# Performance work log

Hardware: AMD Instinct MI355X
Metric: run time of the kernel (lower is better)

## Reference

```python
import jax, jax.numpy as jnp
import numpy as np

B, NQ, NK, D_IN, HD = 1, 16384, 7933, 1024, 512
R = 0.3  # keep-top-r fraction used for the quantile threshold


def _l2norm(x):
    # matches F.normalize(p=2, dim=-1, eps=1e-12)
    n = jnp.linalg.norm(x, axis=-1, keepdims=True)
    return x / jnp.maximum(n, 1e-12)


def setup_inputs() -> dict:
    key = jax.random.key(0)
    ks = jax.random.split(key, 10)
    s = 0.02
    return {
        "query": jax.random.normal(ks[0], (B, NQ, D_IN), jnp.float32),
        "key_x": jax.random.normal(ks[1], (B, NK, D_IN), jnp.float32),
        "wq_w": jax.random.normal(ks[2], (HD, D_IN), jnp.float32) * s,
        "wq_b": jnp.zeros((HD,), jnp.float32),
        "wk_w": jax.random.normal(ks[3], (HD, D_IN), jnp.float32) * s,
        "wk_b": jnp.zeros((HD,), jnp.float32),
        "wa_w": jax.random.normal(ks[4], (1, NK), jnp.float32) * s,
        "wa_b": jnp.zeros((1,), jnp.float32),
        "cls_w": jax.random.normal(ks[5], (1, HD), jnp.float32) * s,
        "cls_b": jnp.zeros((1,), jnp.float32),
    }


def reference(query, key_x, wq_w, wq_b, wk_w, wk_b, wa_w, wa_b, cls_w, cls_b):
    # WQ / WK: Linear + Tanh
    q = jnp.tanh(jnp.einsum("bnd,hd->bnh", query, wq_w) + wq_b)   # [B,NQ,HD]
    k = jnp.tanh(jnp.einsum("bnd,hd->bnh", key_x, wk_w) + wk_b)   # [B,NK,HD]
    # normalized dot-product scores
    A = jnp.einsum("bqh,bkh->bqk", _l2norm(q), _l2norm(k))        # [B,NQ,NK]
    # WA: Linear(NK -> 1)
    A1 = jnp.einsum("bqk,ok->bqo", A, wa_w) + wa_b                # [B,NQ,1]
    # quantile threshold from batch 0 (torch: sorted ascending, index -int(r*NQ))
    thre = jax.lax.stop_gradient(jnp.sort(A1[0, :, 0])[-int(R * NQ)])
    A1 = jnp.where(A1 > thre, A1, 0.0)                            # F.threshold(., thre, 0)
    attn = jax.nn.softmax(A1, axis=1)                             # softmax over NQ (zeros included)
    attn_t = jnp.transpose(attn, (0, 2, 1))                       # [B,1,NQ]
    z = jnp.matmul(attn_t, q).reshape(-1, HD)                     # [B,HD]
    y_prob = z @ cls_w.T + cls_b                                  # [B,1]
    return (y_prob, attn_t)
```

## Files before the change

### kernel.cpp

```cpp
#include <hip/hip_runtime.h>
#include <math.h>

#define NQ 16384
#define NK 7933
#define DI 1024
#define HD 512
#define RANK_TARGET 11469

typedef __bf16 bf16x8 __attribute__((ext_vector_type(8)));
typedef float  f32x4  __attribute__((ext_vector_type(4)));

#define GLOAD_LDS16(g, l)                                                     \
  __builtin_amdgcn_global_load_lds(                                           \
      (const __attribute__((address_space(1))) void*)(g),                     \
      (__attribute__((address_space(3))) void*)(l), 16, 0, 0)

__device__ __forceinline__ unsigned mapf(float f) {
  unsigned b = __float_as_uint(f);
  return (b & 0x80000000u) ? ~b : (b | 0x80000000u);
}

__global__ void conv_all(const float* __restrict__ q, const float* __restrict__ k,
                         const float* __restrict__ wq, const float* __restrict__ wk,
                         __bf16* __restrict__ qbf, __bf16* __restrict__ kbf,
                         __bf16* __restrict__ wqbf, __bf16* __restrict__ wkbf,
                         unsigned* __restrict__ zero_region) {
  if (blockIdx.x == 0) {
    for (int j = threadIdx.x; j < 1088; j += 256) zero_region[j] = 0u;
  }
  const int NQ8 = NQ * DI / 8;
  const int NK8 = NK * DI / 8;
  const int W8  = HD * DI / 8;
  const int total = NQ8 + NK8 + 2 * W8;
  int i = blockIdx.x * blockDim.x + threadIdx.x;
  int stride = gridDim.x * blockDim.x;
  for (; i < total; i += stride) {
    const float* s; __bf16* d; int j;
    if (i < NQ8)                 { s = q;  d = qbf;  j = i; }
    else if (i < NQ8 + NK8)      { s = k;  d = kbf;  j = i - NQ8; }
    else if (i < NQ8 + NK8 + W8) { s = wq; d = wqbf; j = i - NQ8 - NK8; }
    else                         { s = wk; d = wkbf; j = i - NQ8 - NK8 - W8; }
    float4 a = ((const float4*)s)[2 * j];
    float4 b = ((const float4*)s)[2 * j + 1];
    bf16x8 o;
    o[0] = (__bf16)a.x; o[1] = (__bf16)a.y; o[2] = (__bf16)a.z; o[3] = (__bf16)a.w;
    o[4] = (__bf16)b.x; o[5] = (__bf16)b.y; o[6] = (__bf16)b.z; o[7] = (__bf16)b.w;
    ((bf16x8*)d)[j] = o;
  }
}

template <bool FUSE_A1>
__global__ __launch_bounds__(256, 3)
void gemm_bt_tanh(const __bf16* __restrict__ A, const __bf16* __restrict__ B,
                  const float* __restrict__ bias, float* __restrict__ C, int M,
                  const float* __restrict__ v, float* __restrict__ A1dot,
                  float* __restrict__ A1ss) {
  constexpr int K = DI;
  constexpr int N = HD;
  __shared__ __align__(16) __bf16 sA[128 * 64];
  __shared__ __align__(16) __bf16 sB[128 * 64];

  const int tid  = threadIdx.x;
  const int lane = tid & 63;
  const int wave = tid >> 6;
  const int wr = wave >> 1, wc = wave & 1;
  const int m0 = blockIdx.x * 128, n0 = blockIdx.y * 128;

  const int srow = lane >> 3;
  const int scol = (((lane & 7) ^ srow)) << 3;

  const int lrow = lane & 15;
  const int chi  = lane >> 4;

  f32x4 acc[4][4] = {};

  for (int kk = 0; kk < K; kk += 64) {
    __syncthreads();
#pragma unroll
    for (int c = 0; c < 4; ++c) {
      int seg = wave * 4 + c;
      int row = seg * 8 + srow;
      int ga = m0 + row; if (ga > M - 1) ga = M - 1;
      GLOAD_LDS16(A + (size_t)ga * K + kk + scol, &sA[seg * 512]);
      GLOAD_LDS16(B + (size_t)(n0 + row) * K + kk + scol, &sB[seg * 512]);
    }
    __syncthreads();
#pragma unroll
    for (int ks = 0; ks < 64; ks += 32) {
      const int cc = (ks >> 3) + chi;
      const int sw = ((cc ^ (lrow & 7)) << 3);
      bf16x8 af[4], bfr[4];
#pragma unroll
      for (int mi = 0; mi < 4; ++mi)
        af[mi] = *(const bf16x8*)(&sA[(wr * 64 + mi * 16 + lrow) * 64 + sw]);
#pragma unroll
      for (int ni = 0; ni < 4; ++ni)
        bfr[ni] = *(const bf16x8*)(&sB[(wc * 64 + ni * 16 + lrow) * 64 + sw]);
#pragma unroll
      for (int mi = 0; mi < 4; ++mi)
#pragma unroll
        for (int ni = 0; ni < 4; ++ni)
          acc[mi][ni] = __builtin_amdgcn_mfma_f32_16x16x32_bf16(af[mi], bfr[ni], acc[mi][ni], 0, 0, 0);
    }
  }

  const int rbase = m0 + wr * 64 + ((lane >> 4) << 2);
  const int cbase = n0 + wc * 64 + (lane & 15);
  float b4[4], v4[4];
#pragma unroll
  for (int ni = 0; ni < 4; ++ni) {
    b4[ni] = bias[cbase + ni * 16];
    if constexpr (FUSE_A1) v4[ni] = v[cbase + ni * 16];
  }
#pragma unroll
  for (int mi = 0; mi < 4; ++mi) {
#pragma unroll
    for (int r = 0; r < 4; ++r) {
      int grow = rbase + mi * 16 + r;
      if (grow < M) {
        float pd = 0.f, pss = 0.f;
#pragma unroll
        for (int ni = 0; ni < 4; ++ni) {
          float val = tanhf(acc[mi][ni][r] + b4[ni]);
          C[(size_t)grow * N + cbase + ni * 16] = val;
          if constexpr (FUSE_A1) { pd += val * v4[ni]; pss += val * val; }
        }
        if constexpr (FUSE_A1) {
#pragma unroll
          for (int off = 1; off < 16; off <<= 1) {
            pd += __shfl_xor(pd, off);
            pss += __shfl_xor(pss, off);
          }
          if ((lane & 15) == 0) {
            atomicAdd(&A1dot[grow], pd);
            atomicAdd(&A1ss[grow], pss);
          }
        }
      }
    }
  }
}

__global__ __launch_bounds__(256)
void reduce_v_zero(const float* __restrict__ kt, const float* __restrict__ wa,
                   float* __restrict__ v, int M, uint2* __restrict__ zr) {
  {
    int g = blockIdx.x * 256 + threadIdx.x;
    uint2 zz; zz.x = 0u; zz.y = 0u;
    zr[g] = zz;
    if (g < 24576 - 16384) zr[16384 + g] = zz;
  }
  __shared__ float vpart[4][512];
  const int tid = threadIdx.x, lane = tid & 63, wave = tid >> 6;
  const int gw = blockIdx.x * 4 + wave;
  const int tw = gridDim.x * 4;
  float acc[8] = {0, 0, 0, 0, 0, 0, 0, 0};
  for (int r = gw; r < M; r += tw) {
    const float4* p = (const float4*)(kt + (size_t)r * HD + lane * 8);
    float4 x = p[0], y = p[1];
    float ss = x.x * x.x + x.y * x.y + x.z * x.z + x.w * x.w
             + y.x * y.x + y.y * y.y + y.z * y.z + y.w * y.w;
#pragma unroll
    for (int off = 32; off; off >>= 1) ss += __shfl_xor(ss, off);
    float s = wa[r] / fmaxf(sqrtf(ss), 1e-12f);
    acc[0] += s * x.x; acc[1] += s * x.y; acc[2] += s * x.z; acc[3] += s * x.w;
    acc[4] += s * y.x; acc[5] += s * y.y; acc[6] += s * y.z; acc[7] += s * y.w;
  }
#pragma unroll
  for (int j = 0; j < 8; ++j) vpart[wave][lane * 8 + j] = acc[j];
  __syncthreads();
  for (int c = tid; c < 512; c += 256)
    atomicAdd(&v[c], vpart[0][c] + vpart[1][c] + vpart[2][c] + vpart[3][c]);
}

__global__ __launch_bounds__(1024)
void select_kernel(const float* __restrict__ A1dot, const float* __restrict__ A1ss,
                   const float* __restrict__ wa_b, float* __restrict__ A1,
                   unsigned* __restrict__ keyg, float* __restrict__ scf) {
  __shared__ unsigned wred1[16], wred2[16], wred3[16];
  __shared__ unsigned s_res;
  const int t = threadIdx.x, lane = t & 63, wave = t >> 6;
  const float wab = wa_b[0];
  unsigned kloc[16];
#pragma unroll 4
  for (int j = 0; j < 16; ++j) {
    int i = j * 1024 + t;
    float d = A1dot[i], ss = A1ss[i];
    float a1 = d / fmaxf(sqrtf(ss), 1e-12f) + wab;
    A1[i] = a1;
    unsigned k = mapf(a1);
    kloc[j] = k;
    keyg[i] = k;
  }
  if (t == 0) s_res = 0u;
  __syncthreads();

  for (int b = 30; b >= 0; b -= 2) {
    const unsigned res = s_res;
    const unsigned t1 = res | (1u << b);
    const unsigned t2 = res | (2u << b);
    const unsigned t3 = res | (3u << b);
    unsigned c1 = 0, c2 = 0, c3 = 0;
#pragma unroll
    for (int j = 0; j < 16; ++j) {
      unsigned k = kloc[j];
      c1 += (k < t1); c2 += (k < t2); c3 += (k < t3);
    }
#pragma unroll
    for (int off = 32; off; off >>= 1) {
      c1 += __shfl_xor(c1, off);
      c2 += __shfl_xor(c2, off);
      c3 += __shfl_xor(c3, off);
    }
    if (lane == 0) { wred1[wave] = c1; wred2[wave] = c2; wred3[wave] = c3; }
    __syncthreads();
    if (t == 0) {
      unsigned C1 = 0, C2 = 0, C3 = 0;
      for (int w = 0; w < 16; ++w) { C1 += wred1[w]; C2 += wred2[w]; C3 += wred3[w]; }
      unsigned nr = res;
      if (C3 <= RANK_TARGET)      nr = t3;
      else if (C2 <= RANK_TARGET) nr = t2;
      else if (C1 <= RANK_TARGET) nr = t1;
      s_res = nr;
    }
    __syncthreads();
  }
  if (t == 0) {
    unsigned key = s_res;
    unsigned bits = (key & 0x80000000u) ? (key ^ 0x80000000u) : ~key;
    scf[0] = __uint_as_float(bits);
  }
}

__global__ __launch_bounds__(256)
void expz(const float* __restrict__ A1, const float* __restrict__ qt,
          float* __restrict__ scf, float* __restrict__ e_out,
          float* __restrict__ z) {
  __shared__ float vpart[4][512];
  __shared__ float esum[4];
  const int tid = threadIdx.x, lane = tid & 63, wave = tid >> 6;
  const float thre = scf[0];
  const int gw = blockIdx.x * 4 + wave;
  const int tw = gridDim.x * 4;
  float acc[8] = {0, 0, 0, 0, 0, 0, 0, 0};
  float es = 0.f;
  for (int r = gw; r < NQ; r += tw) {
    float x = A1[r]; x = (x > thre) ? x : 0.f;
    float e = expf(x - thre);
    if (lane == 0) e_out[r] = e;
    es += e;
    const float4* p = (const float4*)(qt + (size_t)r * HD + lane * 8);
    float4 u = p[0], w = p[1];
    acc[0] += e * u.x; acc[1] += e * u.y; acc[2] += e * u.z; acc[3] += e * u.w;
    acc[4] += e * w.x; acc[5] += e * w.y; acc[6] += e * w.z; acc[7] += e * w.w;
  }
  if (lane == 0) esum[wave] = es;
#pragma unroll
  for (int j = 0; j < 8; ++j) vpart[wave][lane * 8 + j] = acc[j];
  __syncthreads();
  for (int c = tid; c < 512; c += 256)
    atomicAdd(&z[c], vpart[0][c] + vpart[1][c] + vpart[2][c] + vpart[3][c]);
  if (tid == 0) atomicAdd(&scf[2], esum[0] + esum[1] + esum[2] + esum[3]);
}

__global__ __launch_bounds__(256)
void finalize(float* __restrict__ attn, const float* __restrict__ scf,
              const float* __restrict__ z, const float* __restrict__ cls_w,
              const float* __restrict__ cls_b, float* __restrict__ y) {
  const float invZ = 1.f / scf[2];
  if (blockIdx.x < 64) {
    int i = blockIdx.x * 256 + threadIdx.x;
    attn[i] *= invZ;
  } else if (threadIdx.x < 64) {
    const int lane = threadIdx.x;
    const float4* zp = (const float4*)(z + lane * 8);
    const float4* wp = (const float4*)(cls_w + lane * 8);
    float4 a = zp[0], b = zp[1], c = wp[0], d = wp[1];
    float dot = a.x * c.x + a.y * c.y + a.z * c.z + a.w * c.w
              + b.x * d.x + b.y * d.y + b.z * d.z + b.w * d.w;
#pragma unroll
    for (int off = 32; off; off >>= 1) dot += __shfl_xor(dot, off);
    if (lane == 0) y[0] = dot * invZ + cls_b[0];
  }
}

#define OFF_WQBF 0u
#define OFF_WKBF 1048576u
#define OFF_A1D  1048576u
#define OFF_A1S  1114112u
#define OFF_KEY  1179648u
#define OFF_QBF  2097152u
#define OFF_A1   35651584u
#define OFF_V    35717120u
#define OFF_Z    35719168u
#define OFF_SC   35721216u
#define OFF_KBF  35721472u
#define OFF_KT   51968256u
#define OFF_QT   35721472u

extern "C" void kernel_launch(void* const* d_in, const int* in_sizes, int n_in,
                              void* d_out, int out_size, void* d_ws, size_t ws_size,
                              hipStream_t stream) {
  const float* query = (const float*)d_in[0];
  const float* key_x = (const float*)d_in[1];
  const float* wq_w  = (const float*)d_in[2];
  const float* wq_b  = (const float*)d_in[3];
  const float* wk_w  = (const float*)d_in[4];
  const float* wk_b  = (const float*)d_in[5];
  const float* wa_w  = (const float*)d_in[6];
  const float* wa_b  = (const float*)d_in[7];
  const float* cls_w = (const float*)d_in[8];
  const float* cls_b = (const float*)d_in[9];
  float* out = (float*)d_out;

  char* ws = (char*)d_ws;
  __bf16* wqbf  = (__bf16*)(ws + OFF_WQBF);
  __bf16* wkbf  = (__bf16*)(ws + OFF_WKBF);
  float*  A1dot = (float*)(ws + OFF_A1D);
  float*  A1ss  = (float*)(ws + OFF_A1S);
  unsigned* keyg = (unsigned*)(ws + OFF_KEY);
  __bf16* qbf   = (__bf16*)(ws + OFF_QBF);
  float*  A1    = (float*)(ws + OFF_A1);
  float*  v     = (float*)(ws + OFF_V);
  float*  z     = (float*)(ws + OFF_Z);
  float*  scf   = (float*)(ws + OFF_SC);
  __bf16* kbf   = (__bf16*)(ws + OFF_KBF);
  float*  ktanh = (float*)(ws + OFF_KT);
  float*  qtanh = (float*)(ws + OFF_QT);
  float*  out_attn = out + 1;

  conv_all<<<4096, 256, 0, stream>>>(query, key_x, wq_w, wk_w,
                                     qbf, kbf, wqbf, wkbf, (unsigned*)v);

  gemm_bt_tanh<false><<<dim3(62, 4), 256, 0, stream>>>(
      kbf, wkbf, wk_b, ktanh, NK, nullptr, nullptr, nullptr);

  reduce_v_zero<<<64, 256, 0, stream>>>(ktanh, wa_w, v, NK, (uint2*)A1dot);

  gemm_bt_tanh<true><<<dim3(128, 4), 256, 0, stream>>>(
      qbf, wqbf, wq_b, qtanh, NQ, v, A1dot, A1ss);

  select_kernel<<<1, 1024, 0, stream>>>(A1dot, A1ss, wa_b, A1, keyg, scf);

  expz<<<128, 256, 0, stream>>>(A1, qtanh, scf, out_attn, z);

  finalize<<<65, 256, 0, stream>>>(out_attn, scf, z, cls_w, cls_b, out);
}
```

Baseline: 277.8 us.

## Fuse fp32-to-bf16 activation conversion into GEMM A-tile loads

The separate pass that converted query and key_x to bf16 is removed. Each GEMM now reads the fp32 activations directly, converts them in registers and writes them into swizzled LDS, so only the weights still go through a conversion kernel. The GEMM tile changes to 64x256 with 512 threads, and the expz launch is doubled. This removes a full read and write of the large activation tensors, at the cost of synchronous global loads for the A operand in place of async global-to-LDS copies.

```diff
diff --git a/kernel.cpp b/kernel.cpp
--- a/kernel.cpp
+++ b/kernel.cpp
@@ -20,91 +20,91 @@
   return (b & 0x80000000u) ? ~b : (b | 0x80000000u);
 }
 
-__global__ void conv_all(const float* __restrict__ q, const float* __restrict__ k,
-                         const float* __restrict__ wq, const float* __restrict__ wk,
-                         __bf16* __restrict__ qbf, __bf16* __restrict__ kbf,
-                         __bf16* __restrict__ wqbf, __bf16* __restrict__ wkbf,
-                         unsigned* __restrict__ zero_region) {
+__global__ void conv_w(const float* __restrict__ wq, const float* __restrict__ wk,
+                       __bf16* __restrict__ wqbf, __bf16* __restrict__ wkbf,
+                       unsigned* __restrict__ zero_region) {
   if (blockIdx.x == 0) {
     for (int j = threadIdx.x; j < 1088; j += 256) zero_region[j] = 0u;
   }
-  const int NQ8 = NQ * DI / 8;
-  const int NK8 = NK * DI / 8;
-  const int W8  = HD * DI / 8;
-  const int total = NQ8 + NK8 + 2 * W8;
-  int i = blockIdx.x * blockDim.x + threadIdx.x;
-  int stride = gridDim.x * blockDim.x;
-  for (; i < total; i += stride) {
-    const float* s; __bf16* d; int j;
-    if (i < NQ8)                 { s = q;  d = qbf;  j = i; }
-    else if (i < NQ8 + NK8)      { s = k;  d = kbf;  j = i - NQ8; }
-    else if (i < NQ8 + NK8 + W8) { s = wq; d = wqbf; j = i - NQ8 - NK8; }
-    else                         { s = wk; d = wkbf; j = i - NQ8 - NK8 - W8; }
-    float4 a = ((const float4*)s)[2 * j];
-    float4 b = ((const float4*)s)[2 * j + 1];
-    bf16x8 o;
-    o[0] = (__bf16)a.x; o[1] = (__bf16)a.y; o[2] = (__bf16)a.z; o[3] = (__bf16)a.w;
-    o[4] = (__bf16)b.x; o[5] = (__bf16)b.y; o[6] = (__bf16)b.z; o[7] = (__bf16)b.w;
-    ((bf16x8*)d)[j] = o;
-  }
+  const int W8 = HD * DI / 8;
+  int i = blockIdx.x * 256 + threadIdx.x;
+  const float* s; __bf16* d; int j;
+  if (i < W8) { s = wq; d = wqbf; j = i; }
+  else        { s = wk; d = wkbf; j = i - W8; }
+  float4 a = ((const float4*)s)[2 * j];
+  float4 b = ((const float4*)s)[2 * j + 1];
+  bf16x8 o;
+  o[0] = (__bf16)a.x; o[1] = (__bf16)a.y; o[2] = (__bf16)a.z; o[3] = (__bf16)a.w;
+  o[4] = (__bf16)b.x; o[5] = (__bf16)b.y; o[6] = (__bf16)b.z; o[7] = (__bf16)b.w;
+  ((bf16x8*)d)[j] = o;
 }
 
 template <bool FUSE_A1>
-__global__ __launch_bounds__(256, 3)
-void gemm_bt_tanh(const __bf16* __restrict__ A, const __bf16* __restrict__ B,
-                  const float* __restrict__ bias, float* __restrict__ C, int M,
-                  const float* __restrict__ v, float* __restrict__ A1dot,
-                  float* __restrict__ A1ss) {
+__global__ __launch_bounds__(512, 4)
+void gemm_f32a_tanh(const float* __restrict__ A, const __bf16* __restrict__ B,
+                    const float* __restrict__ bias, float* __restrict__ C, int M,
+                    const float* __restrict__ v, float* __restrict__ A1dot,
+                    float* __restrict__ A1ss) {
   constexpr int K = DI;
   constexpr int N = HD;
-  __shared__ __align__(16) __bf16 sA[128 * 64];
-  __shared__ __align__(16) __bf16 sB[128 * 64];
+  __shared__ __align__(16) __bf16 sA[64 * 64];
+  __shared__ __align__(16) __bf16 sB[256 * 64];
 
   const int tid  = threadIdx.x;
   const int lane = tid & 63;
   const int wave = tid >> 6;
-  const int wr = wave >> 1, wc = wave & 1;
-  const int m0 = blockIdx.x * 128, n0 = blockIdx.y * 128;
+  const int wr = wave >> 2;
+  const int wc = wave & 3;
+  const int m0 = blockIdx.x * 64, n0 = blockIdx.y * 256;
+
+  const int arow = tid >> 3;
+  const int acb  = tid & 7;
+  __bf16* aw = &sA[arow * 64 + ((acb ^ (arow & 7)) << 3)];
+  int ga = m0 + arow; if (ga > M - 1) ga = M - 1;
+  const float* ap = A + (size_t)ga * K + acb * 8;
 
   const int srow = lane >> 3;
-  const int scol = (((lane & 7) ^ srow)) << 3;
+  const int scol = ((lane & 7) ^ srow) << 3;
 
   const int lrow = lane & 15;
   const int chi  = lane >> 4;
 
-  f32x4 acc[4][4] = {};
+  f32x4 acc[2][4] = {};
 
   for (int kk = 0; kk < K; kk += 64) {
+    float4 x0 = *(const float4*)(ap + kk);
+    float4 x1 = *(const float4*)(ap + kk + 4);
     __syncthreads();
+    bf16x8 o;
+    o[0] = (__bf16)x0.x; o[1] = (__bf16)x0.y; o[2] = (__bf16)x0.z; o[3] = (__bf16)x0.w;
+    o[4] = (__bf16)x1.x; o[5] = (__bf16)x1.y; o[6] = (__bf16)x1.z; o[7] = (__bf16)x1.w;
+    *(bf16x8*)aw = o;
 #pragma unroll
     for (int c = 0; c < 4; ++c) {
       int seg = wave * 4 + c;
-      int row = seg * 8 + srow;
-      int ga = m0 + row; if (ga > M - 1) ga = M - 1;
-      GLOAD_LDS16(A + (size_t)ga * K + kk + scol, &sA[seg * 512]);
-      GLOAD_LDS16(B + (size_t)(n0 + row) * K + kk + scol, &sB[seg * 512]);
+      GLOAD_LDS16(B + (size_t)(n0 + seg * 8 + srow) * K + kk + scol, &sB[seg * 512]);
     }
     __syncthreads();
 #pragma unroll
     for (int ks = 0; ks < 64; ks += 32) {
       const int cc = (ks >> 3) + chi;
       const int sw = ((cc ^ (lrow & 7)) << 3);
-      bf16x8 af[4], bfr[4];
-#pragma unroll
-      for (int mi = 0; mi < 4; ++mi)
-        af[mi] = *(const bf16x8*)(&sA[(wr * 64 + mi * 16 + lrow) * 64 + sw]);
+      bf16x8 af[2], bfr[4];
+#pragma unroll
+      for (int mi = 0; mi < 2; ++mi)
+        af[mi] = *(const bf16x8*)(&sA[(wr * 32 + mi * 16 + lrow) * 64 + sw]);
 #pragma unroll
       for (int ni = 0; ni < 4; ++ni)
         bfr[ni] = *(const bf16x8*)(&sB[(wc * 64 + ni * 16 + lrow) * 64 + sw]);
 #pragma unroll
-      for (int mi = 0; mi < 4; ++mi)
+      for (int mi = 0; mi < 2; ++mi)
 #pragma unroll
         for (int ni = 0; ni < 4; ++ni)
           acc[mi][ni] = __builtin_amdgcn_mfma_f32_16x16x32_bf16(af[mi], bfr[ni], acc[mi][ni], 0, 0, 0);
     }
   }
 
-  const int rbase = m0 + wr * 64 + ((lane >> 4) << 2);
+  const int rbase = m0 + wr * 32 + ((lane >> 4) << 2);
   const int cbase = n0 + wc * 64 + (lane & 15);
   float b4[4], v4[4];
 #pragma unroll
@@ -113,7 +113,7 @@
     if constexpr (FUSE_A1) v4[ni] = v[cbase + ni * 16];
   }
 #pragma unroll
-  for (int mi = 0; mi < 4; ++mi) {
+  for (int mi = 0; mi < 2; ++mi) {
 #pragma unroll
     for (int r = 0; r < 4; ++r) {
       int grow = rbase + mi * 16 + r;
@@ -289,12 +289,10 @@
 #define OFF_A1D  1048576u
 #define OFF_A1S  1114112u
 #define OFF_KEY  1179648u
-#define OFF_QBF  2097152u
 #define OFF_A1   35651584u
 #define OFF_V    35717120u
 #define OFF_Z    35719168u
 #define OFF_SC   35721216u
-#define OFF_KBF  35721472u
 #define OFF_KT   51968256u
 #define OFF_QT   35721472u
 
@@ -319,30 +317,27 @@
   float*  A1dot = (float*)(ws + OFF_A1D);
   float*  A1ss  = (float*)(ws + OFF_A1S);
   unsigned* keyg = (unsigned*)(ws + OFF_KEY);
-  __bf16* qbf   = (__bf16*)(ws + OFF_QBF);
   float*  A1    = (float*)(ws + OFF_A1);
   float*  v     = (float*)(ws + OFF_V);
   float*  z     = (float*)(ws + OFF_Z);
   float*  scf   = (float*)(ws + OFF_SC);
-  __bf16* kbf   = (__bf16*)(ws + OFF_KBF);
   float*  ktanh = (float*)(ws + OFF_KT);
   float*  qtanh = (float*)(ws + OFF_QT);
   float*  out_attn = out + 1;
 
-  conv_all<<<4096, 256, 0, stream>>>(query, key_x, wq_w, wk_w,
-                                     qbf, kbf, wqbf, wkbf, (unsigned*)v);
-
-  gemm_bt_tanh<false><<<dim3(62, 4), 256, 0, stream>>>(
-      kbf, wkbf, wk_b, ktanh, NK, nullptr, nullptr, nullptr);
+  conv_w<<<512, 256, 0, stream>>>(wq_w, wk_w, wqbf, wkbf, (unsigned*)v);
+
+  gemm_f32a_tanh<false><<<dim3(124, 2), 512, 0, stream>>>(
+      key_x, wkbf, wk_b, ktanh, NK, nullptr, nullptr, nullptr);
 
   reduce_v_zero<<<64, 256, 0, stream>>>(ktanh, wa_w, v, NK, (uint2*)A1dot);
 
-  gemm_bt_tanh<true><<<dim3(128, 4), 256, 0, stream>>>(
-      qbf, wqbf, wq_b, qtanh, NQ, v, A1dot, A1ss);
+  gemm_f32a_tanh<true><<<dim3(256, 2), 512, 0, stream>>>(
+      query, wqbf, wq_b, qtanh, NQ, v, A1dot, A1ss);
 
   select_kernel<<<1, 1024, 0, stream>>>(A1dot, A1ss, wa_b, A1, keyg, scf);
 
-  expz<<<128, 256, 0, stream>>>(A1, qtanh, scf, out_attn, z);
+  expz<<<256, 256, 0, stream>>>(A1, qtanh, scf, out_attn, z);
 
   finalize<<<65, 256, 0, stream>>>(out_attn, scf, z, cls_w, cls_b, out);
 }
```

Result: faster. 254.2 us (-8.5%).
